# Performance work log

Hardware: AMD Instinct MI355X
Metric: run time of the kernel (lower is better)

Reference implementation:

```python
import jax, jax.numpy as jnp
import numpy as np
import math

FREQS = jnp.array([1., 2., 4., 8., 7., 5.], dtype=jnp.float32)  # default frequencies


def setup_inputs() -> dict:
    key = jax.random.key(0)
    k1, k2, k3 = jax.random.split(key, 3)
    B, N, H, F = 8, 4096, 256, 6
    x = jax.random.normal(k1, (B, N, H), dtype=jnp.float32)
    t = jax.random.uniform(k2, (B, 1), dtype=jnp.float32) * (2.0 * math.pi)
    oscillators = jax.random.normal(k3, (F, H, H), dtype=jnp.float32) * 0.1
    # phase_shifts[i] = i / F * pi, broadcast over hidden dim (matches torch init)
    phase_shifts = jnp.broadcast_to(
        (jnp.arange(F, dtype=jnp.float32) / F * math.pi)[:, None], (F, H)
    ).copy()
    return {"x": x, "t": t, "oscillators": oscillators, "phase_shifts": phase_shifts}


def reference(x, t, oscillators, phase_shifts):
    # resonator[b, f, h] = sin(freq_f * t[b, 0] + phase[f, h])
    res = jnp.sin(FREQS[None, :, None] * t[:, :, None] + phase_shifts[None, :, :])  # [B, F, H]
    # result[b, n, k] = sum_f (x[b, n, :] @ W_f)[k] * res[b, f, k]
    return jnp.einsum('bnh,fhk,bfk->bnk', x, oscillators, res)
```

## Files before the change

kernel.cpp:

```cpp
#include <hip/hip_runtime.h>
#include <hip/hip_bf16.h>


#define B_  8
#define N_  4096
#define H_  256

typedef __attribute__((ext_vector_type(8))) short s8v;
typedef __attribute__((ext_vector_type(4))) float f4v;

#define AS1 __attribute__((address_space(1)))
#define AS3 __attribute__((address_space(3)))
#define GLOAD_LDS16(g, l) \
    __builtin_amdgcn_global_load_lds((const AS1 void*)(g), (AS3 void*)(l), 16, 0, 0)

__global__ __launch_bounds__(256) void build_w(
    const float* __restrict__ osc,
    const float* __restrict__ t,
    const float* __restrict__ phase,
    __hip_bfloat16* __restrict__ Wt)
{
    const float freqs[6] = {1.f, 2.f, 4.f, 8.f, 7.f, 5.f};
    __shared__ float tr[16 * 68];

    const int b  = blockIdx.z;
    const int n0 = blockIdx.y * 64;
    const int h0 = blockIdx.x * 16;
    const int tid = threadIdx.x;

    const float tb = t[b];
    const int nr = (tid & 15) * 4;
    const int hr = tid >> 4;
    float s[6][4];
#pragma unroll
    for (int f = 0; f < 6; ++f)
#pragma unroll
        for (int j = 0; j < 4; ++j)
            s[f][j] = __sinf(freqs[f] * tb + phase[f * 256 + n0 + nr + j]);

    const int h = h0 + hr;
    float4 acc = make_float4(0.f, 0.f, 0.f, 0.f);
#pragma unroll
    for (int f = 0; f < 6; ++f) {
        float4 o = *(const float4*)&osc[f * 65536 + h * 256 + n0 + nr];
        acc.x += o.x * s[f][0];
        acc.y += o.y * s[f][1];
        acc.z += o.z * s[f][2];
        acc.w += o.w * s[f][3];
    }
    *(float4*)&tr[hr * 68 + nr] = acc;
    __syncthreads();

    const int nw = tid >> 2;
    const int hw = (tid & 3) * 4;
    float v0 = tr[(hw + 0) * 68 + nw];
    float v1 = tr[(hw + 1) * 68 + nw];
    float v2 = tr[(hw + 2) * 68 + nw];
    float v3 = tr[(hw + 3) * 68 + nw];
    union { __hip_bfloat162 h2[2]; unsigned long long q; } cv;
    cv.h2[0] = __float22bfloat162_rn(make_float2(v0, v1));
    cv.h2[1] = __float22bfloat162_rn(make_float2(v2, v3));
    *(unsigned long long*)(Wt + (size_t)b * 65536 + (size_t)(n0 + nw) * 256 + h0 + hw) = cv.q;
}

#define LDA 72

__global__ __launch_bounds__(512, 4) void gemm(
    const float* __restrict__ X,
    const __hip_bfloat16* __restrict__ Wt,
    float* __restrict__ out)
{
    __shared__ short As[64 * LDA];
    __shared__ short Bs[2][256 * 64];

    const int b     = blockIdx.y;
    const int mTile = blockIdx.x;

    const int tid    = threadIdx.x;
    const int lane   = tid & 63;
    const int wave   = tid >> 6;
    const int lane15 = lane & 15;
    const int quad   = lane >> 4;
    const int wm     = wave >> 2;
    const int wn     = wave & 3;

    const float* Xb          = X   + (size_t)b * N_ * H_ + (size_t)mTile * 64 * H_;
    const __hip_bfloat16* Wb = Wt  + (size_t)b * H_ * H_;
    float* Ob                = out + (size_t)b * N_ * H_ + (size_t)mTile * 64 * H_;

    const int arow = tid >> 3;
    const int aseg = (tid & 7) * 8;
    const float* pa = Xb + (size_t)arow * H_ + aseg;

    const int brow = lane >> 3;
    const int bK   = lane >> 5;
    const __hip_bfloat16* WbRow = Wb + (size_t)(wave * 32 + brow) * H_;

#define ISSUE_B(buf, kt)                                                      \
    do {                                                                      \
        _Pragma("unroll")                                                     \
        for (int j = 0; j < 4; ++j) {                                         \
            const int csrc = (lane & 7) ^ (j * 2 + bK);                       \
            GLOAD_LDS16(WbRow + (size_t)j * 8 * H_ + (kt) * 64 + csrc * 8,    \
                        &Bs[buf][wave * 2048 + j * 512]);                     \
        }                                                                     \
    } while (0)

    f4v acc[2][4] = {};

    ISSUE_B(0, 0);
    float4 av[2][2];
    av[0][0] = *(const float4*)(pa + 0);
    av[0][1] = *(const float4*)(pa + 4);

#pragma unroll
    for (int it = 0; it < 4; ++it) {
        const int p = it & 1;
        union { __hip_bfloat162 h2[4]; uint4 q; } cv;
        cv.h2[0] = __float22bfloat162_rn(make_float2(av[p][0].x, av[p][0].y));
        cv.h2[1] = __float22bfloat162_rn(make_float2(av[p][0].z, av[p][0].w));
        cv.h2[2] = __float22bfloat162_rn(make_float2(av[p][1].x, av[p][1].y));
        cv.h2[3] = __float22bfloat162_rn(make_float2(av[p][1].z, av[p][1].w));
        *(uint4*)&As[arow * LDA + aseg] = cv.q;

        if (it < 3) {
            ISSUE_B(p ^ 1, it + 1);
            av[p ^ 1][0] = *(const float4*)(pa + (it + 1) * 64);
            av[p ^ 1][1] = *(const float4*)(pa + (it + 1) * 64 + 4);
            asm volatile("s_waitcnt vmcnt(6) lgkmcnt(0)\n\ts_barrier" ::: "memory");
        } else {
            asm volatile("s_waitcnt vmcnt(0) lgkmcnt(0)\n\ts_barrier" ::: "memory");
        }

#pragma unroll
        for (int kh = 0; kh < 2; ++kh) {
            s8v af[2], bf[4];
#pragma unroll
            for (int mt = 0; mt < 2; ++mt)
                af[mt] = *(const s8v*)&As[(wm * 32 + mt * 16 + lane15) * LDA + kh * 32 + quad * 8];
#pragma unroll
            for (int nt = 0; nt < 4; ++nt) {
                const int n  = wn * 64 + lane15 * 4 + nt;
                const int pc = ((kh * 4 + quad) ^ (lane15 & 7)) * 8;
                bf[nt] = *(const s8v*)&Bs[p][n * 64 + pc];
            }
#pragma unroll
            for (int mt = 0; mt < 2; ++mt)
#pragma unroll
                for (int nt = 0; nt < 4; ++nt)
                    acc[mt][nt] = __builtin_amdgcn_mfma_f32_16x16x32_bf16(
                        af[mt], bf[nt], acc[mt][nt], 0, 0, 0);
        }
        if (it < 3)
            asm volatile("s_barrier" ::: "memory");
    }

#pragma unroll
    for (int mt = 0; mt < 2; ++mt) {
#pragma unroll
        for (int r = 0; r < 4; ++r) {
            const int row = wm * 32 + mt * 16 + quad * 4 + r;
            f4v o = { acc[mt][0][r], acc[mt][1][r], acc[mt][2][r], acc[mt][3][r] };
            __builtin_nontemporal_store(o,
                (f4v*)(Ob + (size_t)row * H_ + wn * 64 + lane15 * 4));
        }
    }
}

extern "C" void kernel_launch(void* const* d_in, const int* in_sizes, int n_in,
                              void* d_out, int out_size, void* d_ws, size_t ws_size,
                              hipStream_t stream) {
    const float* x     = (const float*)d_in[0];
    const float* t     = (const float*)d_in[1];
    const float* osc   = (const float*)d_in[2];
    const float* phase = (const float*)d_in[3];
    __hip_bfloat16* Wt = (__hip_bfloat16*)d_ws;
    float* out = (float*)d_out;
    (void)in_sizes; (void)n_in; (void)out_size; (void)ws_size;

    dim3 gw(16, 4, 8);
    build_w<<<gw, 256, 0, stream>>>(osc, t, phase, Wt);

    dim3 gg(64, 8);
    gemm<<<gg, 512, 0, stream>>>(x, Wt, out);
}
```

Before: 93.08 us.

## Fuse W construction into GEMM kernel with per-batch atomic barrier

Removes the separate build_w launch. Each GEMM block first computes one 16x64 tile of the batch's bf16 weight matrix, then all 64 blocks of that batch synchronise through an atomic counter in workspace before loading W. The goal is to save a kernel launch and the gap between the two dependent kernels. In exchange it adds a memset launch per call and a spin-wait grid barrier, which depends on all 512 blocks being co-resident and would deadlock otherwise.

```diff
diff --git a/kernel.cpp b/kernel.cpp
--- a/kernel.cpp
+++ b/kernel.cpp
@@ -14,69 +14,68 @@
 #define GLOAD_LDS16(g, l) \
     __builtin_amdgcn_global_load_lds((const AS1 void*)(g), (AS3 void*)(l), 16, 0, 0)
 
-__global__ __launch_bounds__(256) void build_w(
-    const float* __restrict__ osc,
-    const float* __restrict__ t,
-    const float* __restrict__ phase,
-    __hip_bfloat16* __restrict__ Wt)
-{
-    const float freqs[6] = {1.f, 2.f, 4.f, 8.f, 7.f, 5.f};
-    __shared__ float tr[16 * 68];
-
-    const int b  = blockIdx.z;
-    const int n0 = blockIdx.y * 64;
-    const int h0 = blockIdx.x * 16;
-    const int tid = threadIdx.x;
-
-    const float tb = t[b];
-    const int nr = (tid & 15) * 4;
-    const int hr = tid >> 4;
-    float s[6][4];
-#pragma unroll
-    for (int f = 0; f < 6; ++f)
-#pragma unroll
-        for (int j = 0; j < 4; ++j)
-            s[f][j] = __sinf(freqs[f] * tb + phase[f * 256 + n0 + nr + j]);
-
-    const int h = h0 + hr;
-    float4 acc = make_float4(0.f, 0.f, 0.f, 0.f);
-#pragma unroll
-    for (int f = 0; f < 6; ++f) {
-        float4 o = *(const float4*)&osc[f * 65536 + h * 256 + n0 + nr];
-        acc.x += o.x * s[f][0];
-        acc.y += o.y * s[f][1];
-        acc.z += o.z * s[f][2];
-        acc.w += o.w * s[f][3];
-    }
-    *(float4*)&tr[hr * 68 + nr] = acc;
-    __syncthreads();
-
-    const int nw = tid >> 2;
-    const int hw = (tid & 3) * 4;
-    float v0 = tr[(hw + 0) * 68 + nw];
-    float v1 = tr[(hw + 1) * 68 + nw];
-    float v2 = tr[(hw + 2) * 68 + nw];
-    float v3 = tr[(hw + 3) * 68 + nw];
-    union { __hip_bfloat162 h2[2]; unsigned long long q; } cv;
-    cv.h2[0] = __float22bfloat162_rn(make_float2(v0, v1));
-    cv.h2[1] = __float22bfloat162_rn(make_float2(v2, v3));
-    *(unsigned long long*)(Wt + (size_t)b * 65536 + (size_t)(n0 + nw) * 256 + h0 + hw) = cv.q;
-}
-
 #define LDA 72
 
-__global__ __launch_bounds__(512, 4) void gemm(
+__global__ __launch_bounds__(512, 4) void fused(
     const float* __restrict__ X,
-    const __hip_bfloat16* __restrict__ Wt,
+    const float* __restrict__ t,
+    const float* __restrict__ osc,
+    const float* __restrict__ phase,
+    __hip_bfloat16* Wt,
+    unsigned int* cnt,
     float* __restrict__ out)
 {
+    __shared__ float tr[16 * 68];
     __shared__ short As[64 * LDA];
     __shared__ short Bs[2][256 * 64];
 
+    const int tid = threadIdx.x;
     const int b     = blockIdx.y;
     const int mTile = blockIdx.x;
 
-    const int tid    = threadIdx.x;
+    {
+        const int h0 = (mTile & 15) * 16;
+        const int n0 = ((mTile >> 4) & 3) * 64;
+        if (tid < 256) {
+            const float freqs[6] = {1.f, 2.f, 4.f, 8.f, 7.f, 5.f};
+            const float tb = t[b];
+            const int nr = (tid & 15) * 4;
+            const int hr = tid >> 4;
+            float s[6][4];
+#pragma unroll
+            for (int f = 0; f < 6; ++f)
+#pragma unroll
+                for (int j = 0; j < 4; ++j)
+                    s[f][j] = __sinf(freqs[f] * tb + phase[f * 256 + n0 + nr + j]);
+
+            const int h = h0 + hr;
+            float4 acc = make_float4(0.f, 0.f, 0.f, 0.f);
+#pragma unroll
+            for (int f = 0; f < 6; ++f) {
+                float4 o = *(const float4*)&osc[f * 65536 + h * 256 + n0 + nr];
+                acc.x += o.x * s[f][0];
+                acc.y += o.y * s[f][1];
+                acc.z += o.z * s[f][2];
+                acc.w += o.w * s[f][3];
+            }
+            *(float4*)&tr[hr * 68 + nr] = acc;
+        }
+        __syncthreads();
+        if (tid < 256) {
+            const int nw = tid >> 2;
+            const int hw = (tid & 3) * 4;
+            float v0 = tr[(hw + 0) * 68 + nw];
+            float v1 = tr[(hw + 1) * 68 + nw];
+            float v2 = tr[(hw + 2) * 68 + nw];
+            float v3 = tr[(hw + 3) * 68 + nw];
+            union { __hip_bfloat162 h2[2]; unsigned long long q; } cv;
+            cv.h2[0] = __float22bfloat162_rn(make_float2(v0, v1));
+            cv.h2[1] = __float22bfloat162_rn(make_float2(v2, v3));
+            *(unsigned long long*)(Wt + (size_t)b * 65536 +
+                                   (size_t)(n0 + nw) * 256 + h0 + hw) = cv.q;
+        }
+    }
+
     const int lane   = tid & 63;
     const int wave   = tid >> 6;
     const int lane15 = lane & 15;
@@ -106,12 +105,25 @@
         }                                                                     \
     } while (0)
 
-    f4v acc[2][4] = {};
-
-    ISSUE_B(0, 0);
     float4 av[2][2];
     av[0][0] = *(const float4*)(pa + 0);
     av[0][1] = *(const float4*)(pa + 4);
+
+    __threadfence();
+    __syncthreads();
+    if (tid == 0)
+        __hip_atomic_fetch_add(&cnt[b * 16], 1u,
+                               __ATOMIC_RELEASE, __HIP_MEMORY_SCOPE_AGENT);
+
+    if (lane == 0) {
+        while (__hip_atomic_load(&cnt[b * 16],
+                                 __ATOMIC_RELAXED, __HIP_MEMORY_SCOPE_AGENT) < 64u) {}
+    }
+    __builtin_amdgcn_fence(__ATOMIC_ACQUIRE, "agent");
+    __syncthreads();
+
+    f4v acc[2][4] = {};
+    ISSUE_B(0, 0);
 
 #pragma unroll
     for (int it = 0; it < 4; ++it) {
@@ -175,12 +187,11 @@
     const float* osc   = (const float*)d_in[2];
     const float* phase = (const float*)d_in[3];
     __hip_bfloat16* Wt = (__hip_bfloat16*)d_ws;
+    unsigned int* cnt  = (unsigned int*)((char*)d_ws + (2u << 20));
     float* out = (float*)d_out;
     (void)in_sizes; (void)n_in; (void)out_size; (void)ws_size;
 
-    dim3 gw(16, 4, 8);
-    build_w<<<gw, 256, 0, stream>>>(osc, t, phase, Wt);
+    hipMemsetAsync(cnt, 0, 8 * 16 * sizeof(unsigned int), stream);
 
-    dim3 gg(64, 8);
-    gemm<<<gg, 512, 0, stream>>>(x, Wt, out);
+    fused<<<dim3(64, 8), 512, 0, stream>>>(x, t, osc, phase, Wt, cnt, out);
 }
```

Measured after the change: 231.8 us. 2.49x slower.

## Split GEMM output columns into two tiles per block to raise occupancy

Applied to the files above, without the earlier changes.

The GEMM now splits the 256-wide output into two 128-column tiles along a new grid dimension, so each block stages half of W in LDS. Each wave computes a 16x64 tile instead of 32x64, which halves the accumulator registers. The occupancy hint rises from 4 to 6 blocks. In exchange, each X tile is loaded and converted to bf16 twice, which doubles X read traffic in this memory-bound kernel. The swizzle and the waitcnt count are adjusted for the smaller B loads.

```diff
diff --git a/kernel.cpp b/kernel.cpp
--- a/kernel.cpp
+++ b/kernel.cpp
@@ -65,15 +65,16 @@
 
 #define LDA 72
 
-__global__ __launch_bounds__(512, 4) void gemm(
+__global__ __launch_bounds__(512, 6) void gemm(
     const float* __restrict__ X,
     const __hip_bfloat16* __restrict__ Wt,
     float* __restrict__ out)
 {
     __shared__ short As[64 * LDA];
-    __shared__ short Bs[2][256 * 64];
+    __shared__ short Bs[2][128 * 64];
 
-    const int b     = blockIdx.y;
+    const int b     = blockIdx.z;
+    const int nTile = blockIdx.y;
     const int mTile = blockIdx.x;
 
     const int tid    = threadIdx.x;
@@ -81,12 +82,13 @@
     const int wave   = tid >> 6;
     const int lane15 = lane & 15;
     const int quad   = lane >> 4;
-    const int wm     = wave >> 2;
-    const int wn     = wave & 3;
+    const int wm     = wave >> 1;
+    const int wn     = wave & 1;
 
     const float* Xb          = X   + (size_t)b * N_ * H_ + (size_t)mTile * 64 * H_;
-    const __hip_bfloat16* Wb = Wt  + (size_t)b * H_ * H_;
-    float* Ob                = out + (size_t)b * N_ * H_ + (size_t)mTile * 64 * H_;
+    const __hip_bfloat16* Wb = Wt  + (size_t)b * H_ * H_ + (size_t)nTile * 128 * H_;
+    float* Ob                = out + (size_t)b * N_ * H_ + (size_t)mTile * 64 * H_
+                                   + (size_t)nTile * 128;
 
     const int arow = tid >> 3;
     const int aseg = (tid & 7) * 8;
@@ -94,19 +96,19 @@
 
     const int brow = lane >> 3;
     const int bK   = lane >> 5;
-    const __hip_bfloat16* WbRow = Wb + (size_t)(wave * 32 + brow) * H_;
+    const __hip_bfloat16* WbRow = Wb + (size_t)(wave * 16 + brow) * H_;
 
 #define ISSUE_B(buf, kt)                                                      \
     do {                                                                      \
         _Pragma("unroll")                                                     \
-        for (int j = 0; j < 4; ++j) {                                         \
-            const int csrc = (lane & 7) ^ (j * 2 + bK);                       \
+        for (int j = 0; j < 2; ++j) {                                         \
+            const int csrc = (lane & 7) ^ ((wave & 1) * 4 + j * 2 + bK);      \
             GLOAD_LDS16(WbRow + (size_t)j * 8 * H_ + (kt) * 64 + csrc * 8,    \
-                        &Bs[buf][wave * 2048 + j * 512]);                     \
+                        &Bs[buf][wave * 1024 + j * 512 + 0]);                 \
         }                                                                     \
     } while (0)
 
-    f4v acc[2][4] = {};
+    f4v acc[4] = {};
 
     ISSUE_B(0, 0);
     float4 av[2][2];
@@ -127,17 +129,15 @@
             ISSUE_B(p ^ 1, it + 1);
             av[p ^ 1][0] = *(const float4*)(pa + (it + 1) * 64);
             av[p ^ 1][1] = *(const float4*)(pa + (it + 1) * 64 + 4);
-            asm volatile("s_waitcnt vmcnt(6) lgkmcnt(0)\n\ts_barrier" ::: "memory");
+            asm volatile("s_waitcnt vmcnt(4) lgkmcnt(0)\n\ts_barrier" ::: "memory");
         } else {
             asm volatile("s_waitcnt vmcnt(0) lgkmcnt(0)\n\ts_barrier" ::: "memory");
         }
 
 #pragma unroll
         for (int kh = 0; kh < 2; ++kh) {
-            s8v af[2], bf[4];
-#pragma unroll
-            for (int mt = 0; mt < 2; ++mt)
-                af[mt] = *(const s8v*)&As[(wm * 32 + mt * 16 + lane15) * LDA + kh * 32 + quad * 8];
+            s8v af, bf[4];
+            af = *(const s8v*)&As[(wm * 16 + lane15) * LDA + kh * 32 + quad * 8];
 #pragma unroll
             for (int nt = 0; nt < 4; ++nt) {
                 const int n  = wn * 64 + lane15 * 4 + nt;
@@ -145,25 +145,20 @@
                 bf[nt] = *(const s8v*)&Bs[p][n * 64 + pc];
             }
 #pragma unroll
-            for (int mt = 0; mt < 2; ++mt)
-#pragma unroll
-                for (int nt = 0; nt < 4; ++nt)
-                    acc[mt][nt] = __builtin_amdgcn_mfma_f32_16x16x32_bf16(
-                        af[mt], bf[nt], acc[mt][nt], 0, 0, 0);
+            for (int nt = 0; nt < 4; ++nt)
+                acc[nt] = __builtin_amdgcn_mfma_f32_16x16x32_bf16(
+                    af, bf[nt], acc[nt], 0, 0, 0);
         }
         if (it < 3)
             asm volatile("s_barrier" ::: "memory");
     }
 
 #pragma unroll
-    for (int mt = 0; mt < 2; ++mt) {
-#pragma unroll
-        for (int r = 0; r < 4; ++r) {
-            const int row = wm * 32 + mt * 16 + quad * 4 + r;
-            f4v o = { acc[mt][0][r], acc[mt][1][r], acc[mt][2][r], acc[mt][3][r] };
-            __builtin_nontemporal_store(o,
-                (f4v*)(Ob + (size_t)row * H_ + wn * 64 + lane15 * 4));
-        }
+    for (int r = 0; r < 4; ++r) {
+        const int row = wm * 16 + quad * 4 + r;
+        f4v o = { acc[0][r], acc[1][r], acc[2][r], acc[3][r] };
+        __builtin_nontemporal_store(o,
+            (f4v*)(Ob + (size_t)row * H_ + wn * 64 + lane15 * 4));
     }
 }
 
@@ -181,6 +176,6 @@
     dim3 gw(16, 4, 8);
     build_w<<<gw, 256, 0, stream>>>(osc, t, phase, Wt);
 
-    dim3 gg(64, 8);
+    dim3 gg(64, 2, 8);
     gemm<<<gg, 512, 0, stream>>>(x, Wt, out);
 }
```

Measured after the change: 93.44 us. About the same (+0.4%).
